# Kernel tuning notes

Hardware: AMD Instinct MI355X
Metric: run time of the kernel (lower is better)

The kernel has to match this reference:

```python
import jax, jax.numpy as jnp
import numpy as np
from jax import lax

EPS = 1e-5
DILATION = 1

def setup_inputs() -> dict:
    key = jax.random.key(0)
    k1, k2, k3 = jax.random.split(key, 3)
    B, C, T, K = 32, 384, 8192, 3
    inp = jax.random.normal(k1, (B, C, T), dtype=jnp.float32)
    # depthwise conv kernel [C, 1, K] (groups=C), kaiming-ish scale
    weight = jax.random.normal(k2, (C, 1, K), dtype=jnp.float32) * (1.0 / np.sqrt(K))
    bias = jax.random.normal(k3, (C,), dtype=jnp.float32) * 0.01
    return {"inp": inp, "weight": weight, "bias": bias}

def reference(inp, weight, bias):
    # InstanceNorm1d: per-(batch, channel) normalization over time, no affine
    mean = jnp.mean(inp, axis=-1, keepdims=True)
    var = jnp.var(inp, axis=-1, keepdims=True)
    x = (inp - mean) * lax.rsqrt(var + EPS)
    # ELU activation
    x = jax.nn.elu(x)
    # depthwise dilated Conv1d, padding=dilation keeps length (ksz=3)
    C = inp.shape[1]
    y = lax.conv_general_dilated(
        x, weight,
        window_strides=(1,),
        padding=[(DILATION, DILATION)],
        rhs_dilation=(DILATION,),
        dimension_numbers=("NCH", "OIH", "NCH"),
        feature_group_count=C,
    )
    y = y + bias[None, :, None]
    # residual add
    return y + inp
```

## Files before the change

### kernel.cpp

```cpp
#include <hip/hip_runtime.h>
#include <math.h>


constexpr int T_LEN = 8192;
constexpr int C_CH  = 384;
constexpr int BLOCK = 256;
constexpr int VPT   = T_LEN / (BLOCK * 4);
constexpr float EPS = 1e-5f;

__device__ __forceinline__ float elu_f(float x) {
    return x > 0.0f ? x : expm1f(x);
}

__global__ __launch_bounds__(BLOCK)
void tcn_resblock_kernel(const float* __restrict__ inp,
                         const float* __restrict__ weight,
                         const float* __restrict__ bias,
                         float* __restrict__ out) {
    __shared__ float s_row[T_LEN];
    __shared__ float s_red[8];

    const int row = blockIdx.x;
    const int c   = row % C_CH;
    const float* __restrict__ in_row  = inp + (size_t)row * T_LEN;
    float* __restrict__       out_row = out + (size_t)row * T_LEN;

    const int tid = threadIdx.x;

    float4 raw[VPT];
    float sum = 0.0f, sumsq = 0.0f;
#pragma unroll
    for (int k = 0; k < VPT; ++k) {
        const int idx = (k * BLOCK + tid) * 4;
        float4 v = *reinterpret_cast<const float4*>(in_row + idx);
        raw[k] = v;
        *reinterpret_cast<float4*>(s_row + idx) = v;
        sum   += (v.x + v.y) + (v.z + v.w);
        sumsq += (v.x * v.x + v.y * v.y) + (v.z * v.z + v.w * v.w);
    }

#pragma unroll
    for (int off = 32; off > 0; off >>= 1) {
        sum   += __shfl_down(sum,   off, 64);
        sumsq += __shfl_down(sumsq, off, 64);
    }
    const int wave = tid >> 6;
    if ((tid & 63) == 0) {
        s_red[wave * 2]     = sum;
        s_red[wave * 2 + 1] = sumsq;
    }
    __syncthreads();

    const float tot   = (s_red[0] + s_red[2]) + (s_red[4] + s_red[6]);
    const float totsq = (s_red[1] + s_red[3]) + (s_red[5] + s_red[7]);
    const float inv_t = 1.0f / (float)T_LEN;
    const float mean  = tot * inv_t;
    const float var   = totsq * inv_t - mean * mean;
    const float rstd  = rsqrtf(var + EPS);

    const float w0 = weight[c * 3 + 0];
    const float w1 = weight[c * 3 + 1];
    const float w2 = weight[c * 3 + 2];
    const float bi = bias[c];

#pragma unroll
    for (int k = 0; k < VPT; ++k) {
        const int idx = (k * BLOCK + tid) * 4;
        const float4 v = raw[k];
        const float e0 = elu_f((v.x - mean) * rstd);
        const float e1 = elu_f((v.y - mean) * rstd);
        const float e2 = elu_f((v.z - mean) * rstd);
        const float e3 = elu_f((v.w - mean) * rstd);

        float el = 0.0f, er = 0.0f;
        if (idx != 0)
            el = elu_f((s_row[idx - 1] - mean) * rstd);
        if (idx + 4 != T_LEN)
            er = elu_f((s_row[idx + 4] - mean) * rstd);

        float4 o;
        o.x = w0 * el + w1 * e0 + w2 * e1 + bi + v.x;
        o.y = w0 * e0 + w1 * e1 + w2 * e2 + bi + v.y;
        o.z = w0 * e1 + w1 * e2 + w2 * e3 + bi + v.z;
        o.w = w0 * e2 + w1 * e3 + w2 * er + bi + v.w;
        *reinterpret_cast<float4*>(out_row + idx) = o;
    }
}

extern "C" void kernel_launch(void* const* d_in, const int* in_sizes, int n_in,
                              void* d_out, int out_size, void* d_ws, size_t ws_size,
                              hipStream_t stream) {
    const float* inp    = (const float*)d_in[0];
    const float* weight = (const float*)d_in[1];
    const float* bias   = (const float*)d_in[2];
    float* out          = (float*)d_out;

    const int rows = in_sizes[0] / T_LEN;
    tcn_resblock_kernel<<<rows, BLOCK, 0, stream>>>(inp, weight, bias, out);
}
```

Before: 642.1 us.

## Replace shared-memory row staging with wave shuffles for conv halo

Drops the 32KB shared-memory copy of each row and gets the neighbour ELU values through intra-wave shuffles. Only wave-boundary edge values are stored in a small shared array. This frees LDS, so more blocks can be resident per CU, and removes the LDS write and read traffic. It also adds nontemporal loads and stores, a fast __expf-based ELU in place of expm1f, and FMA-folded normalization. The exp-minus-one form loses some precision near zero.

Result: faster. 622.1 us (-3.1%).

```diff
diff --git a/kernel.cpp b/kernel.cpp
--- a/kernel.cpp
+++ b/kernel.cpp
@@ -1,15 +1,18 @@
 #include <hip/hip_runtime.h>
 #include <math.h>
 
+
+typedef float f32x4 __attribute__((ext_vector_type(4)));
 
 constexpr int T_LEN = 8192;
 constexpr int C_CH  = 384;
 constexpr int BLOCK = 256;
 constexpr int VPT   = T_LEN / (BLOCK * 4);
+constexpr int WAVES = BLOCK / 64;
 constexpr float EPS = 1e-5f;
 
-__device__ __forceinline__ float elu_f(float x) {
-    return x > 0.0f ? x : expm1f(x);
+__device__ __forceinline__ float elu_fast(float x) {
+    return x > 0.0f ? x : (__expf(x) - 1.0f);
 }
 
 __global__ __launch_bounds__(BLOCK)
@@ -17,35 +20,44 @@
                          const float* __restrict__ weight,
                          const float* __restrict__ bias,
                          float* __restrict__ out) {
-    __shared__ float s_row[T_LEN];
-    __shared__ float s_red[8];
+    __shared__ float s_red[WAVES * 2];
+    __shared__ float s_lx[WAVES][VPT];
+    __shared__ float s_lw[WAVES][VPT];
 
     const int row = blockIdx.x;
     const int c   = row % C_CH;
     const float* __restrict__ in_row  = inp + (size_t)row * T_LEN;
     float* __restrict__       out_row = out + (size_t)row * T_LEN;
 
-    const int tid = threadIdx.x;
+    const int tid  = threadIdx.x;
+    const int lane = tid & 63;
+    const int wave = tid >> 6;
 
-    float4 raw[VPT];
+    f32x4 raw[VPT];
     float sum = 0.0f, sumsq = 0.0f;
 #pragma unroll
     for (int k = 0; k < VPT; ++k) {
         const int idx = (k * BLOCK + tid) * 4;
-        float4 v = *reinterpret_cast<const float4*>(in_row + idx);
+        f32x4 v = __builtin_nontemporal_load(
+            reinterpret_cast<const f32x4*>(in_row + idx));
         raw[k] = v;
-        *reinterpret_cast<float4*>(s_row + idx) = v;
         sum   += (v.x + v.y) + (v.z + v.w);
-        sumsq += (v.x * v.x + v.y * v.y) + (v.z * v.z + v.w * v.w);
+        sumsq += fmaf(v.x, v.x, fmaf(v.y, v.y, fmaf(v.z, v.z, v.w * v.w)));
+        if (lane == 0)  s_lx[wave][k] = v.x;
+        if (lane == 63) s_lw[wave][k] = v.w;
     }
+
+    const float w0 = weight[c * 3 + 0];
+    const float w1 = weight[c * 3 + 1];
+    const float w2 = weight[c * 3 + 2];
+    const float bi = bias[c];
 
 #pragma unroll
     for (int off = 32; off > 0; off >>= 1) {
         sum   += __shfl_down(sum,   off, 64);
         sumsq += __shfl_down(sumsq, off, 64);
     }
-    const int wave = tid >> 6;
-    if ((tid & 63) == 0) {
+    if (lane == 0) {
         s_red[wave * 2]     = sum;
         s_red[wave * 2 + 1] = sumsq;
     }
@@ -57,33 +69,45 @@
     const float mean  = tot * inv_t;
     const float var   = totsq * inv_t - mean * mean;
     const float rstd  = rsqrtf(var + EPS);
-
-    const float w0 = weight[c * 3 + 0];
-    const float w1 = weight[c * 3 + 1];
-    const float w2 = weight[c * 3 + 2];
-    const float bi = bias[c];
+    const float nms   = -mean * rstd;
 
 #pragma unroll
     for (int k = 0; k < VPT; ++k) {
         const int idx = (k * BLOCK + tid) * 4;
-        const float4 v = raw[k];
-        const float e0 = elu_f((v.x - mean) * rstd);
-        const float e1 = elu_f((v.y - mean) * rstd);
-        const float e2 = elu_f((v.z - mean) * rstd);
-        const float e3 = elu_f((v.w - mean) * rstd);
+        const f32x4 v = raw[k];
+        const float e0 = elu_fast(fmaf(v.x, rstd, nms));
+        const float e1 = elu_fast(fmaf(v.y, rstd, nms));
+        const float e2 = elu_fast(fmaf(v.z, rstd, nms));
+        const float e3 = elu_fast(fmaf(v.w, rstd, nms));
 
-        float el = 0.0f, er = 0.0f;
-        if (idx != 0)
-            el = elu_f((s_row[idx - 1] - mean) * rstd);
-        if (idx + 4 != T_LEN)
-            er = elu_f((s_row[idx + 4] - mean) * rstd);
+        float el = __shfl_up(e3, 1, 64);
+        if (lane == 0) {
+            if (wave == 0 && k == 0) {
+                el = 0.0f;
+            } else {
+                const float lraw = (wave == 0) ? s_lw[WAVES - 1][k - 1]
+                                               : s_lw[wave - 1][k];
+                el = elu_fast(fmaf(lraw, rstd, nms));
+            }
+        }
+        float er = __shfl_down(e0, 1, 64);
+        if (lane == 63) {
+            if (wave == WAVES - 1 && k == VPT - 1) {
+                er = 0.0f;
+            } else {
+                const float rraw = (wave == WAVES - 1) ? s_lx[0][k + 1]
+                                                       : s_lx[wave + 1][k];
+                er = elu_fast(fmaf(rraw, rstd, nms));
+            }
+        }
 
-        float4 o;
-        o.x = w0 * el + w1 * e0 + w2 * e1 + bi + v.x;
-        o.y = w0 * e0 + w1 * e1 + w2 * e2 + bi + v.y;
-        o.z = w0 * e1 + w1 * e2 + w2 * e3 + bi + v.z;
-        o.w = w0 * e2 + w1 * e3 + w2 * er + bi + v.w;
-        *reinterpret_cast<float4*>(out_row + idx) = o;
+        f32x4 o;
+        o.x = fmaf(w0, el, fmaf(w1, e0, fmaf(w2, e1, bi))) + v.x;
+        o.y = fmaf(w0, e0, fmaf(w1, e1, fmaf(w2, e2, bi))) + v.y;
+        o.z = fmaf(w0, e1, fmaf(w1, e2, fmaf(w2, e3, bi))) + v.z;
+        o.w = fmaf(w0, e2, fmaf(w1, e3, fmaf(w2, er, bi))) + v.w;
+        __builtin_nontemporal_store(o,
+            reinterpret_cast<f32x4*>(out_row + idx));
     }
 }
 
```
